# Kernel optimization log

Measured on AMD Instinct MI355X. Metric: run time of the kernel, lower is better.

## Reference

```python
import jax, jax.numpy as jnp
import numpy as np

K, D = 8, 4
LOG2PI = float(np.log(2.0 * np.pi))
TRIL_ROWS, TRIL_COLS = np.tril_indices(D)


def setup_inputs() -> dict:
    key = jax.random.key(0)
    k1, k2 = jax.random.split(key)
    M = 512
    B = 4096
    phi_dim = K + K * D + K * D * (D + 1) // 2  # 120
    phi = jax.random.normal(k1, (M, phi_dim), dtype=jnp.float32)
    X_ref = jax.random.normal(k2, (B, D), dtype=jnp.float32)
    return {"phi": phi, "X_ref": X_ref}


def reference(phi, X_ref):
    M = phi.shape[0]
    B = X_ref.shape[0]
    # unpack_phi: [pi_tilde | mu | L_vecs]
    pi_tilde = phi[:, :K]                                   # [M, K]
    mu = phi[:, K:K + K * D].reshape(M, K, D)               # [M, K, D]
    L_vecs = phi[:, K + K * D:].reshape(M, K, D * (D + 1) // 2)
    # L_vec_to_matrix: lower-triangular fill (row-major tril order)
    L = jnp.zeros((M, K, D, D), phi.dtype).at[:, :, TRIL_ROWS, TRIL_COLS].set(L_vecs)
    pi = jax.nn.softmax(pi_tilde, axis=-1)                  # [M, K]

    # --- mean responsibilities (GMM E-step) ---
    diff = X_ref[None, None, :, :] - mu[:, :, None, :]      # [M, K, B, D]
    L_flat = L.reshape(M * K, D, D)
    diff_flat = jnp.transpose(diff.reshape(M * K, B, D), (0, 2, 1))  # [MK, D, B]
    alpha = jax.scipy.linalg.solve_triangular(L_flat, diff_flat, lower=True)
    maha = (alpha ** 2).sum(1).reshape(M, K, B)             # Mahalanobis distances
    log_det = 2.0 * jnp.log(
        jnp.clip(jnp.abs(jnp.diagonal(L_flat, axis1=-2, axis2=-1)), 1e-8)
    ).sum(-1).reshape(M, K)
    log_norm = -0.5 * (D * LOG2PI + log_det[:, :, None])
    log_gauss = log_norm - 0.5 * maha                       # [M, K, B]
    log_joint = jnp.log(jnp.clip(pi, 1e-8))[:, :, None] + log_gauss
    log_resp = log_joint - jax.scipy.special.logsumexp(log_joint, axis=1, keepdims=True)
    resp = jnp.exp(log_resp).mean(-1)                       # [M, K]

    # --- combined embedding: [mu | log|diag L| | pi | resp] ---
    mu_flat = mu.reshape(M, K * D)
    L_diag = jnp.diagonal(L, axis1=-2, axis2=-1)            # [M, K, D]
    log_L_flat = jnp.log(jnp.clip(jnp.abs(L_diag), 1e-6)).reshape(M, K * D)
    z = jnp.concatenate([mu_flat, log_L_flat, pi, resp], axis=-1)

    # per-feature standardization across particles (torch.std => ddof=1)
    mean = z.mean(axis=0, keepdims=True)
    std = jnp.clip(z.std(axis=0, ddof=1, keepdims=True), 1e-6)
    return (z - mean) / std
```

## Files before the change

kernel.cpp:

```cpp
#include <hip/hip_runtime.h>
#include <math.h>

#define KK 8
#define LOG2E  1.4426950408889634f
#define HL2E   0.7213475204444817f
#define LOG2PI 1.8378770664093453f

__global__ __launch_bounds__(256) void gmm_main(const float* __restrict__ phi,
                                                const float* __restrict__ X,
                                                float* __restrict__ z) {
    __shared__ float4 sp[KK][4];
    __shared__ float swr[4][KK];

    const int b = blockIdx.x;
    const int m = b >> 2;
    const int sub = b & 3;
    const int t = threadIdx.x;
    const float* row = phi + m * 120;

    if (t < KK) {
        float mx = row[0];
        #pragma unroll
        for (int j = 1; j < KK; ++j) mx = fmaxf(mx, row[j]);
        float s = 0.f;
        #pragma unroll
        for (int j = 0; j < KK; ++j) s += __expf(row[j] - mx);
        float pik = __expf(row[t] - mx) / s;
        if (sub == 0) z[m * 80 + 64 + t] = pik;

        const float* muk = row + 8 + t * 4;
        const float* Lv  = row + 40 + t * 10;
        float l00 = Lv[0], l10 = Lv[1], l11 = Lv[2], l20 = Lv[3], l21 = Lv[4],
              l22 = Lv[5], l30 = Lv[6], l31 = Lv[7], l32 = Lv[8], l33 = Lv[9];
        float i0 = 1.f / l00, i1 = 1.f / l11, i2 = 1.f / l22, i3 = 1.f / l33;
        float w00 = i0;
        float w10 = -i1 * l10 * w00;
        float w11 = i1;
        float w20 = -i2 * (l20 * w00 + l21 * w10);
        float w21 = -i2 * (l21 * w11);
        float w22 = i2;
        float w30 = -i3 * (l30 * w00 + l31 * w10 + l32 * w20);
        float w31 = -i3 * (l31 * w11 + l32 * w21);
        float w32 = -i3 * (l32 * w22);
        float w33 = i3;
        float logdet = 2.f * (__logf(fmaxf(fabsf(l00), 1e-8f)) +
                              __logf(fmaxf(fabsf(l11), 1e-8f)) +
                              __logf(fmaxf(fabsf(l22), 1e-8f)) +
                              __logf(fmaxf(fabsf(l33), 1e-8f)));
        float c2 = (__logf(fmaxf(pik, 1e-8f)) -
                    0.5f * (4.f * LOG2PI + logdet)) * LOG2E;
        sp[t][0] = make_float4(muk[0], muk[1], muk[2], muk[3]);
        sp[t][1] = make_float4(w00, w10, w11, w20);
        sp[t][2] = make_float4(w21, w22, w30, w31);
        sp[t][3] = make_float4(w32, w33, c2, 0.f);
    } else if (sub == 0 && t >= 64 && t < 96) {
        int j = t - 64;
        z[m * 80 + j] = row[8 + j];
    } else if (sub == 0 && t >= 96 && t < 128) {
        int j = t - 96, k = j >> 2, d = j & 3;
        int didx = (d == 0) ? 0 : (d == 1) ? 2 : (d == 2) ? 5 : 9;
        z[m * 80 + 32 + j] = __logf(fmaxf(fabsf(row[40 + k * 10 + didx]), 1e-6f));
    }
    __syncthreads();

    float acc[KK];
    #pragma unroll
    for (int k = 0; k < KK; ++k) acc[k] = 0.f;

    const float4* X4 = reinterpret_cast<const float4*>(X);
    float4 xv[4];
    #pragma unroll
    for (int i = 0; i < 4; ++i) xv[i] = X4[sub * 1024 + i * 256 + t];

    float lj[4][KK];
    #pragma unroll
    for (int k = 0; k < KK; ++k) {
        float4 p0 = sp[k][0], p1 = sp[k][1], p2 = sp[k][2], p3 = sp[k][3];
        #pragma unroll
        for (int i = 0; i < 4; ++i) {
            float d0 = xv[i].x - p0.x;
            float d1 = xv[i].y - p0.y;
            float d2 = xv[i].z - p0.z;
            float d3 = xv[i].w - p0.w;
            float a0 = d0 * p1.x;
            float a1 = fmaf(p1.y, d0, d1 * p1.z);
            float a2 = fmaf(p1.w, d0, fmaf(p2.x, d1, d2 * p2.y));
            float a3 = fmaf(p2.z, d0, fmaf(p2.w, d1, fmaf(p3.x, d2, d3 * p3.y)));
            float sq = fmaf(a0, a0, fmaf(a1, a1, fmaf(a2, a2, a3 * a3)));
            lj[i][k] = fmaf(-HL2E, sq, p3.z);
        }
    }
    #pragma unroll
    for (int i = 0; i < 4; ++i) {
        float mx = lj[i][0];
        #pragma unroll
        for (int k = 1; k < KK; ++k) mx = fmaxf(mx, lj[i][k]);
        float e[KK], s = 0.f;
        #pragma unroll
        for (int k = 0; k < KK; ++k) {
            e[k] = __builtin_amdgcn_exp2f(lj[i][k] - mx);
            s += e[k];
        }
        float inv = __builtin_amdgcn_rcpf(s);
        #pragma unroll
        for (int k = 0; k < KK; ++k) acc[k] = fmaf(e[k], inv, acc[k]);
    }

    #pragma unroll
    for (int k = 0; k < KK; ++k) {
        float v = acc[k];
        #pragma unroll
        for (int off = 32; off; off >>= 1) v += __shfl_xor(v, off, 64);
        acc[k] = v;
    }
    if ((t & 63) == 0) {
        int wid = t >> 6;
        #pragma unroll
        for (int k = 0; k < KK; ++k) swr[wid][k] = acc[k];
    }
    __syncthreads();
    if (t < KK) {
        float s = swr[0][t] + swr[1][t] + swr[2][t] + swr[3][t];
        atomicAdd(&z[m * 80 + 72 + t], s);
    }
}

__global__ __launch_bounds__(512) void gmm_norm(float* __restrict__ z, int M) {
    __shared__ float sw[8];
    const int col = blockIdx.x;
    const int t = threadIdx.x;

    float v = z[t * 80 + col];

    float r = v;
    #pragma unroll
    for (int off = 32; off; off >>= 1) r += __shfl_xor(r, off, 64);
    if ((t & 63) == 0) sw[t >> 6] = r;
    __syncthreads();
    float tot = 0.f;
    #pragma unroll
    for (int w = 0; w < 8; ++w) tot += sw[w];
    float mean = tot / (float)M;
    __syncthreads();

    float d = v - mean;
    r = d * d;
    #pragma unroll
    for (int off = 32; off; off >>= 1) r += __shfl_xor(r, off, 64);
    if ((t & 63) == 0) sw[t >> 6] = r;
    __syncthreads();
    float tot2 = 0.f;
    #pragma unroll
    for (int w = 0; w < 8; ++w) tot2 += sw[w];
    float stdv = fmaxf(sqrtf(tot2 / (float)(M - 1)), 1e-6f);

    z[t * 80 + col] = d / stdv;
}

extern "C" void kernel_launch(void* const* d_in, const int* in_sizes, int n_in,
                              void* d_out, int out_size, void* d_ws, size_t ws_size,
                              hipStream_t stream) {
    const float* phi = (const float*)d_in[0];
    const float* X   = (const float*)d_in[1];
    const int M = in_sizes[0] / 120;
    float* z = (float*)d_out;

    hipMemsetAsync(z, 0, (size_t)out_size * sizeof(float), stream);
    gmm_main<<<M * 4, 256, 0, stream>>>(phi, X, z);
    gmm_norm<<<80, 512, 0, stream>>>(z, M);
}
```

Measured before the change: 72.02 us.

## Remove memset, atomics and block barriers by per-wave parameter setup and workspace partials

Each wave now computes its own copy of the per-component Gaussian parameters in its own shared-memory slot, so the block-level __syncthreads calls disappear. Each wave writes its partial responsibilities to a workspace instead of atomically adding into the output, which removes the memset launch and the atomics. The normalization kernel now recomputes the mu, log-diagonal and softmax columns straight from phi and sums the 16 partials per particle. The cost is redundant parameter setup in every wave, and the code assumes wave-synchronous visibility of shared memory within a wave without an explicit barrier.

Result: slower. 73.94 us (+2.7%).

```diff
diff --git a/kernel.cpp b/kernel.cpp
--- a/kernel.cpp
+++ b/kernel.cpp
@@ -2,34 +2,44 @@
 #include <math.h>
 
 #define KK 8
-#define LOG2E  1.4426950408889634f
-#define HL2E   0.7213475204444817f
-#define LOG2PI 1.8378770664093453f
+#define LOG2E   1.4426950408889634f
+#define HL2E    0.7213475204444817f
+#define LN2     0.6931471805599453f
+#define LOG2PI  1.8378770664093453f
+#define C2CONST 5.3029936094f
+#define L2CLIP8 -26.575424759f
 
 __global__ __launch_bounds__(256) void gmm_main(const float* __restrict__ phi,
                                                 const float* __restrict__ X,
-                                                float* __restrict__ z) {
-    __shared__ float4 sp[KK][4];
-    __shared__ float swr[4][KK];
+                                                float* __restrict__ ws) {
+    __shared__ float4 sp[4][KK][4];
 
     const int b = blockIdx.x;
     const int m = b >> 2;
     const int sub = b & 3;
     const int t = threadIdx.x;
+    const int w = t >> 6;
+    const int lane = t & 63;
     const float* row = phi + m * 120;
 
-    if (t < KK) {
+    const float4* X4 = reinterpret_cast<const float4*>(X);
+    float4 xv[4];
+    #pragma unroll
+    for (int i = 0; i < 4; ++i) xv[i] = X4[sub * 1024 + w * 256 + i * 64 + lane];
+
+    if (lane < KK) {
         float mx = row[0];
         #pragma unroll
         for (int j = 1; j < KK; ++j) mx = fmaxf(mx, row[j]);
         float s = 0.f;
         #pragma unroll
-        for (int j = 0; j < KK; ++j) s += __expf(row[j] - mx);
-        float pik = __expf(row[t] - mx) / s;
-        if (sub == 0) z[m * 80 + 64 + t] = pik;
+        for (int j = 0; j < KK; ++j)
+            s += __builtin_amdgcn_exp2f((row[j] - mx) * LOG2E);
+        float l2pi = fmaxf((row[lane] - mx) * LOG2E - __builtin_amdgcn_logf(s),
+                           L2CLIP8);
 
-        const float* muk = row + 8 + t * 4;
-        const float* Lv  = row + 40 + t * 10;
+        const float* muk = row + 8 + lane * 4;
+        const float* Lv  = row + 40 + lane * 10;
         float l00 = Lv[0], l10 = Lv[1], l11 = Lv[2], l20 = Lv[3], l21 = Lv[4],
               l22 = Lv[5], l30 = Lv[6], l31 = Lv[7], l32 = Lv[8], l33 = Lv[9];
         float i0 = 1.f / l00, i1 = 1.f / l11, i2 = 1.f / l22, i3 = 1.f / l33;
@@ -43,39 +53,26 @@
         float w31 = -i3 * (l31 * w11 + l32 * w21);
         float w32 = -i3 * (l32 * w22);
         float w33 = i3;
-        float logdet = 2.f * (__logf(fmaxf(fabsf(l00), 1e-8f)) +
-                              __logf(fmaxf(fabsf(l11), 1e-8f)) +
-                              __logf(fmaxf(fabsf(l22), 1e-8f)) +
-                              __logf(fmaxf(fabsf(l33), 1e-8f)));
-        float c2 = (__logf(fmaxf(pik, 1e-8f)) -
-                    0.5f * (4.f * LOG2PI + logdet)) * LOG2E;
-        sp[t][0] = make_float4(muk[0], muk[1], muk[2], muk[3]);
-        sp[t][1] = make_float4(w00, w10, w11, w20);
-        sp[t][2] = make_float4(w21, w22, w30, w31);
-        sp[t][3] = make_float4(w32, w33, c2, 0.f);
-    } else if (sub == 0 && t >= 64 && t < 96) {
-        int j = t - 64;
-        z[m * 80 + j] = row[8 + j];
-    } else if (sub == 0 && t >= 96 && t < 128) {
-        int j = t - 96, k = j >> 2, d = j & 3;
-        int didx = (d == 0) ? 0 : (d == 1) ? 2 : (d == 2) ? 5 : 9;
-        z[m * 80 + 32 + j] = __logf(fmaxf(fabsf(row[40 + k * 10 + didx]), 1e-6f));
+        float sl = __builtin_amdgcn_logf(fmaxf(fabsf(l00), 1e-8f)) +
+                   __builtin_amdgcn_logf(fmaxf(fabsf(l11), 1e-8f)) +
+                   __builtin_amdgcn_logf(fmaxf(fabsf(l22), 1e-8f)) +
+                   __builtin_amdgcn_logf(fmaxf(fabsf(l33), 1e-8f));
+        float c2 = l2pi - C2CONST - sl;
+        sp[w][lane][0] = make_float4(muk[0], muk[1], muk[2], muk[3]);
+        sp[w][lane][1] = make_float4(w00, w10, w11, w20);
+        sp[w][lane][2] = make_float4(w21, w22, w30, w31);
+        sp[w][lane][3] = make_float4(w32, w33, c2, 0.f);
     }
-    __syncthreads();
 
     float acc[KK];
     #pragma unroll
     for (int k = 0; k < KK; ++k) acc[k] = 0.f;
 
-    const float4* X4 = reinterpret_cast<const float4*>(X);
-    float4 xv[4];
-    #pragma unroll
-    for (int i = 0; i < 4; ++i) xv[i] = X4[sub * 1024 + i * 256 + t];
-
     float lj[4][KK];
     #pragma unroll
     for (int k = 0; k < KK; ++k) {
-        float4 p0 = sp[k][0], p1 = sp[k][1], p2 = sp[k][2], p3 = sp[k][3];
+        float4 p0 = sp[w][k][0], p1 = sp[w][k][1],
+               p2 = sp[w][k][2], p3 = sp[w][k][3];
         #pragma unroll
         for (int i = 0; i < 4; ++i) {
             float d0 = xv[i].x - p0.x;
@@ -113,24 +110,44 @@
         for (int off = 32; off; off >>= 1) v += __shfl_xor(v, off, 64);
         acc[k] = v;
     }
-    if ((t & 63) == 0) {
-        int wid = t >> 6;
-        #pragma unroll
-        for (int k = 0; k < KK; ++k) swr[wid][k] = acc[k];
-    }
-    __syncthreads();
-    if (t < KK) {
-        float s = swr[0][t] + swr[1][t] + swr[2][t] + swr[3][t];
-        atomicAdd(&z[m * 80 + 72 + t], s);
+    if (lane < KK) {
+        int p = m * 16 + sub * 4 + w;
+        ws[p * 8 + lane] = acc[lane];
     }
 }
 
-__global__ __launch_bounds__(512) void gmm_norm(float* __restrict__ z, int M) {
+__global__ __launch_bounds__(512) void gmm_norm(const float* __restrict__ phi,
+                                                const float* __restrict__ ws,
+                                                float* __restrict__ out, int M) {
     __shared__ float sw[8];
     const int col = blockIdx.x;
     const int t = threadIdx.x;
+    const float* row = phi + t * 120;
 
-    float v = z[t * 80 + col];
+    float v;
+    if (col < 32) {
+        v = row[8 + col];
+    } else if (col < 64) {
+        int j = col - 32, k = j >> 2, d = j & 3;
+        int didx = (d == 0) ? 0 : (d == 1) ? 2 : (d == 2) ? 5 : 9;
+        v = __builtin_amdgcn_logf(fmaxf(fabsf(row[40 + k * 10 + didx]), 1e-6f)) * LN2;
+    } else if (col < 72) {
+        int k = col - 64;
+        float mx = row[0];
+        #pragma unroll
+        for (int j = 1; j < KK; ++j) mx = fmaxf(mx, row[j]);
+        float s = 0.f;
+        #pragma unroll
+        for (int j = 0; j < KK; ++j)
+            s += __builtin_amdgcn_exp2f((row[j] - mx) * LOG2E);
+        v = __builtin_amdgcn_exp2f((row[k] - mx) * LOG2E) *
+            __builtin_amdgcn_rcpf(s);
+    } else {
+        int k = col - 72;
+        v = 0.f;
+        #pragma unroll
+        for (int q = 0; q < 16; ++q) v += ws[(t * 16 + q) * 8 + k];
+    }
 
     float r = v;
     #pragma unroll
@@ -154,7 +171,7 @@
     for (int w = 0; w < 8; ++w) tot2 += sw[w];
     float stdv = fmaxf(sqrtf(tot2 / (float)(M - 1)), 1e-6f);
 
-    z[t * 80 + col] = d / stdv;
+    out[t * 80 + col] = d / stdv;
 }
 
 extern "C" void kernel_launch(void* const* d_in, const int* in_sizes, int n_in,
@@ -163,9 +180,8 @@
     const float* phi = (const float*)d_in[0];
     const float* X   = (const float*)d_in[1];
     const int M = in_sizes[0] / 120;
-    float* z = (float*)d_out;
+    float* ws = (float*)d_ws;
 
-    hipMemsetAsync(z, 0, (size_t)out_size * sizeof(float), stream);
-    gmm_main<<<M * 4, 256, 0, stream>>>(phi, X, z);
-    gmm_norm<<<80, 512, 0, stream>>>(z, M);
+    gmm_main<<<M * 4, 256, 0, stream>>>(phi, X, ws);
+    gmm_norm<<<80, 512, 0, stream>>>(phi, ws, (float*)d_out, M);
 }
```
